# Kernel optimization log

Measured on AMD Instinct MI355X. Metric: run time of the kernel, lower is better.

## Reference

```python
import jax, jax.numpy as jnp
import numpy as np

N, E, T, D, C = 20000, 160000, 3, 128, 128  # nodes, edges, replicas, in=out feat dim, num_classes
NUM_EDGES = 128  # linear1 output width (must be <= C for the H scatter to be in-range)


def setup_inputs() -> dict:
    key = jax.random.key(0)
    ks = jax.random.split(key, 8)
    s = 1.0 / np.sqrt(D)
    return {
        "edge_index": jax.random.randint(ks[0], (2, E), 0, N, dtype=jnp.int32),
        "features": jax.random.normal(ks[1], (N, D), jnp.float32),
        "lin_W": jax.random.normal(ks[2], (T, D, D), jnp.float32) * s,   # t per-replica Linears
        "lin_b": jnp.zeros((T, D), jnp.float32),
        "gcn1_W": jax.random.normal(ks[3], (D, C), jnp.float32) * s,
        "gcn1_b": jnp.zeros((C,), jnp.float32),
        "gcn2_W": jax.random.normal(ks[4], (C, C), jnp.float32) * s,
        "gcn2_b": jnp.zeros((C,), jnp.float32),
        "lin1_W": jax.random.normal(ks[5], (C, NUM_EDGES), jnp.float32) * s,
        "lin1_b": jnp.zeros((NUM_EDGES,), jnp.float32),
    }


def _gcn(x, W, b, src, dst, n):
    """PyG GCNConv: add self-loops, symmetric deg^-1/2 normalization, scatter-add."""
    loop = jnp.arange(n, dtype=src.dtype)
    src = jnp.concatenate([src, loop])
    dst = jnp.concatenate([dst, loop])
    deg = jax.ops.segment_sum(jnp.ones(src.shape, x.dtype), dst, num_segments=n)
    dinv = jax.lax.rsqrt(deg)  # deg >= 1 because of self-loops
    norm = dinv[src] * dinv[dst]
    xw = x @ W
    return jax.ops.segment_sum(xw[src] * norm[:, None], dst, num_segments=n) + b


def reference(edge_index, features, lin_W, lin_b, gcn1_W, gcn1_b, gcn2_W, gcn2_b, lin1_W, lin1_b):
    src, dst = edge_index[0], edge_index[1]
    n = features.shape[0]
    t = lin_W.shape[0]
    scale = features.shape[1] ** -0.5  # out_features ** -0.5
    # t linear replicas, concatenated along nodes -> [t*n, D]
    transformed = (jnp.einsum('nd,tde->tne', features, lin_W) + lin_b[:, None, :]).reshape(t * n, -1)
    # replicate-selection via cosine similarity (exact torch index order:
    # src.repeat_interleave(t) vs dst.repeat(t))
    rep_src = jnp.repeat(src, t)
    exp_dst = jnp.tile(dst, t)
    a = features[rep_src]
    bb = transformed[exp_dst]
    sim = (a * bb).sum(-1) / jnp.maximum(
        jnp.linalg.norm(a, axis=-1) * jnp.linalg.norm(bb, axis=-1), 1e-8)
    best = jnp.argmax(sim.reshape(-1, t), axis=1)            # [E]
    best_nodes = dst + best.astype(dst.dtype) * n            # index into replica blocks
    # extra edges: (arange(n), arange(n) + i*n) for i in range(t)
    extra_src = jnp.tile(jnp.arange(n, dtype=src.dtype), t)
    extra_dst = (jnp.arange(n, dtype=src.dtype)[None, :]
                 + (jnp.arange(t, dtype=src.dtype) * n)[:, None]).reshape(-1)
    src_all = jnp.concatenate([src, src, extra_src])
    dst_all = jnp.concatenate([dst, best_nodes, extra_dst])
    nt = (t + 1) * n
    all_features = jnp.concatenate([features, transformed], axis=0)  # [(t+1)n, D]
    # GCN backbone (dropout = identity in eval mode)
    h = jax.nn.relu(all_features)
    h = jax.nn.relu(_gcn(h, gcn1_W, gcn1_b, src_all, dst_all, nt))
    all_features2 = _gcn(h, gcn2_W, gcn2_b, src_all, dst_all, nt)    # [(t+1)n, C]
    logits = jax.nn.relu(all_features2) @ lin1_W + lin1_b            # [(t+1)n, NUM_EDGES]
    num_classes = gcn2_b.shape[0]
    classes = jnp.argmax(logits.reshape(t + 1, n, -1), axis=-1)      # [t+1, n]
    H = jax.nn.one_hot(classes, num_classes, dtype=features.dtype).sum(0)  # [n, C] vote counts
    # per-class segment sum over nodes with H[:, j] > 0 (only first n rows are ever selected)
    mask = (H > 0).astype(features.dtype)                            # [n, C]
    hyperedge_features = mask.T @ all_features2[:n]                  # [C, D]
    dots = (all_features @ hyperedge_features.T) * scale             # [(t+1)n, C]
    H = jax.nn.softmax(H, axis=0)
    return H, hyperedge_features, dots
```

## Files before the change

kernel.cpp:

```cpp
#include <hip/hip_runtime.h>
#include <math.h>

#define NN 20000
#define NE 160000
#define TT 3
#define DD 128
#define NTOT 80000
#define N3 60000
#define NBLK1 79

__device__ __forceinline__ float waveReduceSum(float v) {
#pragma unroll
  for (int off = 32; off >= 1; off >>= 1)
    v += __shfl_xor(v, off, 64);
  return v;
}

__device__ __forceinline__ void atomAddF(float* p, float v) {
  unsafeAtomicAdd(p, v);
}

__global__ __launch_bounds__(256) void k_copy_feat(const float* __restrict__ src,
                                                   float* __restrict__ dst, int n4) {
  int i = blockIdx.x * 256 + threadIdx.x;
  if (i < n4) ((float4*)dst)[i] = ((const float4*)src)[i];
}

template <int RELU_IN, int TRANS_W, int DO_ARGMAX>
__global__ __launch_bounds__(512, 4) void gemm128(const float* __restrict__ X,
                                                  const float* __restrict__ W,
                                                  const float* __restrict__ bias,
                                                  float* __restrict__ out, int M,
                                                  float scale, int wStride, int bStride,
                                                  long oStride, int* __restrict__ cls) {
  __shared__ float Ws[128 * 132];
  const int tid = threadIdx.x;
  const int rbase = blockIdx.x * 160;
  W += (long)blockIdx.y * wStride;
  if (bias) bias += (long)blockIdx.y * bStride;
  out += (long)blockIdx.y * oStride;

#pragma unroll
  for (int it = 0; it < 8; ++it) {
    int idx = (tid + it * 512) * 4;
    int kl = idx >> 7, c = idx & 127;
    float4 w;
    if (!TRANS_W) {
      w = *(const float4*)&W[kl * 128 + c];
    } else {
      w.x = W[(c + 0) * 128 + kl];
      w.y = W[(c + 1) * 128 + kl];
      w.z = W[(c + 2) * 128 + kl];
      w.w = W[(c + 3) * 128 + kl];
    }
    *(float4*)&Ws[kl * 132 + c] = w;
  }

  const int tc = tid & 15, tr = tid >> 4;
  const int c0 = tc * 8, r0 = tr * 5;

  const float4* xrow[5];
#pragma unroll
  for (int i = 0; i < 5; ++i) {
    int gr = rbase + r0 + i;
    int gc = (gr < M) ? gr : 0;
    xrow[i] = (const float4*)(X + (long)gc * 128);
  }

  float acc[5][8];
#pragma unroll
  for (int i = 0; i < 5; ++i)
#pragma unroll
    for (int j = 0; j < 8; ++j) acc[i][j] = 0.f;

  float4 xc[5], xn[5];
#pragma unroll
  for (int i = 0; i < 5; ++i) {
    float4 v = xrow[i][0];
    if (RELU_IN) {
      v.x = fmaxf(v.x, 0.f);
      v.y = fmaxf(v.y, 0.f);
      v.z = fmaxf(v.z, 0.f);
      v.w = fmaxf(v.w, 0.f);
    }
    xc[i] = v;
  }

  __syncthreads();

  for (int kq = 0; kq < 32; ++kq) {
    if (kq < 31) {
#pragma unroll
      for (int i = 0; i < 5; ++i) {
        float4 v = xrow[i][kq + 1];
        if (RELU_IN) {
          v.x = fmaxf(v.x, 0.f);
          v.y = fmaxf(v.y, 0.f);
          v.z = fmaxf(v.z, 0.f);
          v.w = fmaxf(v.w, 0.f);
        }
        xn[i] = v;
      }
    }
    const int klb = kq * 4;
#pragma unroll
    for (int k = 0; k < 4; ++k) {
      const int kl = klb + k;
      const float4 wa = *(const float4*)&Ws[kl * 132 + c0];
      const float4 wb = *(const float4*)&Ws[kl * 132 + c0 + 4];
      float av[5];
#pragma unroll
      for (int i = 0; i < 5; ++i)
        av[i] = (k == 0) ? xc[i].x : (k == 1) ? xc[i].y : (k == 2) ? xc[i].z : xc[i].w;
      const float bv[8] = {wa.x, wa.y, wa.z, wa.w, wb.x, wb.y, wb.z, wb.w};
#pragma unroll
      for (int i = 0; i < 5; ++i)
#pragma unroll
        for (int j = 0; j < 8; ++j) acc[i][j] = fmaf(av[i], bv[j], acc[i][j]);
    }
    if (kq < 31) {
#pragma unroll
      for (int i = 0; i < 5; ++i) xc[i] = xn[i];
    }
  }

  float bb[8];
#pragma unroll
  for (int j = 0; j < 8; ++j) bb[j] = 0.f;
  if (bias) {
#pragma unroll
    for (int j = 0; j < 8; ++j) bb[j] = bias[c0 + j];
  }

  if (DO_ARGMAX) {
#pragma unroll
    for (int i = 0; i < 5; ++i) {
      float bv = acc[i][0] * scale + bb[0];
      int bc = c0;
#pragma unroll
      for (int j = 1; j < 8; ++j) {
        float v = acc[i][j] * scale + bb[j];
        if (v > bv) {
          bv = v;
          bc = c0 + j;
        }
      }
#pragma unroll
      for (int off = 1; off <= 8; off <<= 1) {
        float ov = __shfl_xor(bv, off, 64);
        int oc = __shfl_xor(bc, off, 64);
        if (ov > bv || (ov == bv && oc < bc)) {
          bv = ov;
          bc = oc;
        }
      }
      int gr = rbase + r0 + i;
      if (tc == 0 && gr < M) cls[gr] = bc;
    }
  } else {
#pragma unroll
    for (int i = 0; i < 5; ++i) {
      int gr = rbase + r0 + i;
      if (gr < M) {
        float4 v0, v1;
        v0.x = acc[i][0] * scale + bb[0];
        v0.y = acc[i][1] * scale + bb[1];
        v0.z = acc[i][2] * scale + bb[2];
        v0.w = acc[i][3] * scale + bb[3];
        v1.x = acc[i][4] * scale + bb[4];
        v1.y = acc[i][5] * scale + bb[5];
        v1.z = acc[i][6] * scale + bb[6];
        v1.w = acc[i][7] * scale + bb[7];
        *(float4*)&out[(long)gr * 128 + c0] = v0;
        *(float4*)&out[(long)gr * 128 + c0 + 4] = v1;
      }
    }
  }
}

__global__ __launch_bounds__(256) void k_norms(const float* __restrict__ feat,
                                               const float* __restrict__ A,
                                               float* __restrict__ nf,
                                               float* __restrict__ nt0) {
  int w = blockIdx.x * 4 + (threadIdx.x >> 6);
  int lane = threadIdx.x & 63;
  if (w >= 2 * NN) return;
  const float* p = (w < NN) ? (feat + (long)w * 128) : (A + (long)(NN + (w - NN)) * 128);
  float2 v = *(const float2*)(p + lane * 2);
  float s = waveReduceSum(v.x * v.x + v.y * v.y);
  if (lane == 0) {
    float r = sqrtf(s);
    if (w < NN) nf[w] = r;
    else nt0[w - NN] = r;
  }
}

__global__ __launch_bounds__(256) void k_sim(const int* __restrict__ ei,
                                             const float* __restrict__ feat,
                                             const float* __restrict__ A,
                                             const float* __restrict__ nf,
                                             const float* __restrict__ nt0,
                                             int* __restrict__ bn) {
  int e = blockIdx.x * 4 + (threadIdx.x >> 6);
  int lane = threadIdx.x & 63;
  if (e >= NE) return;
  int s = ei[e];
  float2 a = *(const float2*)(feat + (long)s * 128 + lane * 2);
  float na = nf[s];
  int dd[3];
#pragma unroll
  for (int k = 0; k < 3; ++k) {
    int j = 3 * e + k;
    if (j >= NE) j -= NE;
    if (j >= NE) j -= NE;
    dd[k] = ei[NE + j];
  }
  float2 b0 = *(const float2*)(A + (long)(NN + dd[0]) * 128 + lane * 2);
  float2 b1 = *(const float2*)(A + (long)(NN + dd[1]) * 128 + lane * 2);
  float2 b2 = *(const float2*)(A + (long)(NN + dd[2]) * 128 + lane * 2);
  float s0 = waveReduceSum(a.x * b0.x + a.y * b0.y);
  float s1 = waveReduceSum(a.x * b1.x + a.y * b1.y);
  float s2 = waveReduceSum(a.x * b2.x + a.y * b2.y);
  float sim0 = s0 / fmaxf(na * nt0[dd[0]], 1e-8f);
  float sim1 = s1 / fmaxf(na * nt0[dd[1]], 1e-8f);
  float sim2 = s2 / fmaxf(na * nt0[dd[2]], 1e-8f);
  int bk = 0;
  float bv = sim0;
  if (sim1 > bv) {
    bv = sim1;
    bk = 1;
  }
  if (sim2 > bv) {
    bv = sim2;
    bk = 2;
  }
  if (lane == 0) bn[e] = ei[NE + e] + bk * NN;
}

__global__ __launch_bounds__(256) void k_zero_count(int* __restrict__ count) {
  int v = blockIdx.x * 256 + threadIdx.x;
  if (v < NTOT) count[v] = 0;
}

__global__ __launch_bounds__(256) void k_count(const int* __restrict__ ei,
                                               const int* __restrict__ bn,
                                               int* __restrict__ count) {
  int e = blockIdx.x * 256 + threadIdx.x;
  if (e < NE) {
    atomicAdd(&count[ei[NE + e]], 1);
    atomicAdd(&count[bn[e]], 1);
  }
}

__global__ __launch_bounds__(256) void k_dinv(const int* __restrict__ count,
                                              float* __restrict__ dinv) {
  int v = blockIdx.x * 256 + threadIdx.x;
  if (v < NTOT) {
    float deg = (float)count[v] + ((v < N3) ? 2.f : 1.f);
    dinv[v] = 1.f / sqrtf(deg);
  }
}

__global__ __launch_bounds__(256) void k_scan1(const int* __restrict__ count,
                                               int* __restrict__ start,
                                               int* __restrict__ bsum) {
  __shared__ int sh[256];
  const int b = blockIdx.x, t = threadIdx.x;
  const int base = b * 1024 + t * 4;
  int c[4];
  int s = 0;
#pragma unroll
  for (int k = 0; k < 4; ++k) {
    int idx = base + k;
    c[k] = (idx < NTOT) ? count[idx] : 0;
    s += c[k];
  }
  sh[t] = s;
  __syncthreads();
  for (int off = 1; off < 256; off <<= 1) {
    int v = (t >= off) ? sh[t - off] : 0;
    __syncthreads();
    sh[t] += v;
    __syncthreads();
  }
  if (t == 255) bsum[b] = sh[255];
  int run = sh[t] - s;
#pragma unroll
  for (int k = 0; k < 4; ++k) {
    int idx = base + k;
    if (idx < NTOT) start[idx] = run;
    run += c[k];
  }
}

__global__ __launch_bounds__(256) void k_scan2(int* __restrict__ bsum) {
  __shared__ int sh[256];
  const int t = threadIdx.x;
  int v = (t < NBLK1) ? bsum[t] : 0;
  sh[t] = v;
  __syncthreads();
  for (int off = 1; off < 256; off <<= 1) {
    int u = (t >= off) ? sh[t - off] : 0;
    __syncthreads();
    sh[t] += u;
    __syncthreads();
  }
  if (t < NBLK1) bsum[t] = sh[t] - v;
}

__global__ __launch_bounds__(256) void k_scan3(int* __restrict__ start,
                                               const int* __restrict__ bsum,
                                               int* __restrict__ cursor) {
  int i = blockIdx.x * 256 + threadIdx.x;
  if (i < NTOT) {
    int v = start[i] + bsum[i >> 10];
    start[i] = v;
    cursor[i] = v;
  }
}

__global__ __launch_bounds__(256) void k_fill(const int* __restrict__ ei,
                                              const int* __restrict__ bn,
                                              const float* __restrict__ dinv,
                                              int* __restrict__ cursor,
                                              int2* __restrict__ ent) {
  int g = blockIdx.x * 256 + threadIdx.x;
  if (g >= 2 * NE) return;
  int e = (g < NE) ? g : g - NE;
  int s = ei[e];
  int d = (g < NE) ? ei[NE + e] : bn[e];
  float w = dinv[s] * dinv[d];
  int pos = atomicAdd(&cursor[d], 1);
  ent[pos] = make_int2(s, __float_as_int(w));
}

__global__ __launch_bounds__(256) void k_agg(const int2* __restrict__ ent,
                                             const int* __restrict__ start,
                                             const int* __restrict__ end,
                                             const float* __restrict__ xw,
                                             const float* __restrict__ dinv,
                                             const float* __restrict__ bias,
                                             float* __restrict__ out) {
  int v = blockIdx.x * 4 + (threadIdx.x >> 6);
  int lane = threadIdx.x & 63;
  float dv = dinv[v];
  float2 xv = *(const float2*)(xw + (long)v * 128 + lane * 2);
  float2 b2 = *(const float2*)(bias + lane * 2);
  float acc0 = b2.x + dv * dv * xv.x;
  float acc1 = b2.y + dv * dv * xv.y;
  if (v < NN) {
    acc0 += dv * dv * xv.x;
    acc1 += dv * dv * xv.y;
  } else if (v < N3) {
    int j = (v < 2 * NN) ? v - NN : v - 2 * NN;
    float2 xj = *(const float2*)(xw + (long)j * 128 + lane * 2);
    float w = dinv[j] * dv;
    acc0 = fmaf(w, xj.x, acc0);
    acc1 = fmaf(w, xj.y, acc1);
  }
  const int i1 = end[v];
  int i = start[v];
  for (; i + 1 < i1; i += 2) {
    int2 e0 = ent[i], e1 = ent[i + 1];
    float w0 = __int_as_float(e0.y), w1 = __int_as_float(e1.y);
    float2 x0 = *(const float2*)(xw + (long)e0.x * 128 + lane * 2);
    float2 x1 = *(const float2*)(xw + (long)e1.x * 128 + lane * 2);
    acc0 = fmaf(w0, x0.x, acc0);
    acc1 = fmaf(w0, x0.y, acc1);
    acc0 = fmaf(w1, x1.x, acc0);
    acc1 = fmaf(w1, x1.y, acc1);
  }
  if (i < i1) {
    int2 e0 = ent[i];
    float w0 = __int_as_float(e0.y);
    float2 x0 = *(const float2*)(xw + (long)e0.x * 128 + lane * 2);
    acc0 = fmaf(w0, x0.x, acc0);
    acc1 = fmaf(w0, x0.y, acc1);
  }
  *(float2*)(out + (long)v * 128 + lane * 2) = make_float2(acc0, acc1);
}

__global__ __launch_bounds__(256) void k_zero_small(float* __restrict__ hyper,
                                                    int* __restrict__ hist) {
  int i = blockIdx.x * 256 + threadIdx.x;
  if (i < 128 * 128) hyper[i] = 0.f;
  if (i < 640) hist[i] = 0;
}

#define HISTBLK 20
__global__ __launch_bounds__(256) void k_hist(const int* __restrict__ cls,
                                              int* __restrict__ hist) {
  __shared__ int sh[640];
  const int t = threadIdx.x;
  for (int i = t; i < 640; i += 256) sh[i] = 0;
  __syncthreads();
  const int per = NN / HISTBLK;
  const int j0 = blockIdx.x * per;
  for (int j = j0 + t; j < j0 + per; j += 256) {
    int cc[4] = {cls[j], cls[NN + j], cls[2 * NN + j], cls[3 * NN + j]};
#pragma unroll
    for (int i = 0; i < 4; ++i) {
      bool first = true;
      int m = 0;
#pragma unroll
      for (int k = 0; k < 4; ++k) {
        if (cc[k] == cc[i]) {
          if (k < i) first = false;
          m++;
        }
      }
      if (first) atomicAdd(&sh[cc[i] * 5 + m], 1);
    }
  }
  __syncthreads();
  for (int i = t; i < 640; i += 256) {
    int v = sh[i];
    if (v) atomicAdd(&hist[i], v);
  }
}

__global__ void k_table(const int* __restrict__ hist, float* __restrict__ table) {
  int c = threadIdx.x;
  if (c >= 128) return;
  int cnt[5];
  int tot = 0;
  for (int v = 1; v <= 4; ++v) {
    cnt[v] = hist[c * 5 + v];
    tot += cnt[v];
  }
  cnt[0] = NN - tot;
  int m = 0;
  for (int v = 0; v <= 4; ++v)
    if (cnt[v] > 0) m = v;
  float ex[5];
  float denom = 0.f;
  for (int v = 0; v <= 4; ++v) {
    ex[v] = expf((float)(v - m));
    denom += (float)cnt[v] * ex[v];
  }
  for (int v = 0; v <= 4; ++v) table[c * 5 + v] = ex[v] / denom;
}

__global__ __launch_bounds__(256) void k_hwrite(const int* __restrict__ cls,
                                                const float* __restrict__ table,
                                                float* __restrict__ H) {
  int j = blockIdx.x * 2 + (threadIdx.x >> 7);
  int c = threadIdx.x & 127;
  if (j >= NN) return;
  int c0 = cls[j], c1 = cls[NN + j], c2 = cls[2 * NN + j], c3 = cls[3 * NN + j];
  int cnt = (c == c0) + (c == c1) + (c == c2) + (c == c3);
  H[(long)j * 128 + c] = table[c * 5 + cnt];
}

#define HBLK 250
#define HPER 80
__global__ __launch_bounds__(256) void k_hyper(const int* __restrict__ cls,
                                               const float* __restrict__ af2,
                                               float* __restrict__ hyper) {
  __shared__ float acc[128 * 128];
  const int t = threadIdx.x;
  for (int i = t; i < 128 * 128; i += 256) acc[i] = 0.f;
  __syncthreads();
  const int j0 = blockIdx.x * HPER;
  const int j1 = j0 + HPER;
  const int d = t & 127;
  const int half = t >> 7;
  float v = af2[(long)j0 * 128 + d];
  int c0 = cls[j0], c1 = cls[NN + j0], c2 = cls[2 * NN + j0], c3 = cls[3 * NN + j0];
  for (int j = j0; j < j1; ++j) {
    float vn = 0.f;
    int n0 = 0, n1 = 0, n2 = 0, n3 = 0;
    if (j + 1 < j1) {
      vn = af2[(long)(j + 1) * 128 + d];
      n0 = cls[j + 1];
      n1 = cls[NN + j + 1];
      n2 = cls[2 * NN + j + 1];
      n3 = cls[3 * NN + j + 1];
    }
    if (half == 0) {
      atomicAdd(&acc[c0 * 128 + d], v);
      if (c2 != c0 && c2 != c1) atomicAdd(&acc[c2 * 128 + d], v);
    } else {
      if (c1 != c0) atomicAdd(&acc[c1 * 128 + d], v);
      if (c3 != c0 && c3 != c1 && c3 != c2) atomicAdd(&acc[c3 * 128 + d], v);
    }
    v = vn;
    c0 = n0;
    c1 = n1;
    c2 = n2;
    c3 = n3;
  }
  __syncthreads();
  for (int i = t; i < 128 * 128; i += 256) {
    float x = acc[i];
    if (x != 0.f) atomAddF(&hyper[i], x);
  }
}

extern "C" void kernel_launch(void* const* d_in, const int* in_sizes, int n_in,
                              void* d_out, int out_size, void* d_ws, size_t ws_size,
                              hipStream_t stream) {
  (void)in_sizes;
  (void)n_in;
  (void)out_size;
  (void)ws_size;
  const int* ei = (const int*)d_in[0];
  const float* feat = (const float*)d_in[1];
  const float* lin_W = (const float*)d_in[2];
  const float* lin_b = (const float*)d_in[3];
  const float* g1W = (const float*)d_in[4];
  const float* g1b = (const float*)d_in[5];
  const float* g2W = (const float*)d_in[6];
  const float* g2b = (const float*)d_in[7];
  const float* l1W = (const float*)d_in[8];
  const float* l1b = (const float*)d_in[9];

  float* out = (float*)d_out;
  float* H = out;
  float* hyper = out + (size_t)NN * 128;
  float* dots = hyper + 128 * 128;

  float* ws = (float*)d_ws;
  float* A = ws;
  float* Cb = A + (size_t)NTOT * 128;
  float* Bb = dots;
  float* dinv = Cb + (size_t)NTOT * 128;
  float* nf = dinv + NTOT;
  float* nt0 = nf + NN;
  int* bn = (int*)(nt0 + NN);
  int* cls = bn + NE;
  int* hist = cls + NTOT;
  float* table = (float*)(hist + 640);
  int* count = (int*)(table + 640);
  int* startA = count + NTOT;
  int* cursor = startA + NTOT;
  int* bsum = cursor + NTOT;
  int2* ent = (int2*)(bsum + 128);

  const float kScale = 0.08838834764831843f;

  k_copy_feat<<<(NN * 128 / 4 + 255) / 256, 256, 0, stream>>>(feat, A, NN * 128 / 4);
  gemm128<0, 0, 0><<<dim3(125, 3), 512, 0, stream>>>(
      feat, lin_W, lin_b, A + (size_t)NN * 128, NN, 1.f, 128 * 128, 128,
      (long)NN * 128, nullptr);
  k_norms<<<10000, 256, 0, stream>>>(feat, A, nf, nt0);
  k_zero_count<<<(NTOT + 255) / 256, 256, 0, stream>>>(count);
  k_sim<<<NE / 4, 256, 0, stream>>>(ei, feat, A, nf, nt0, bn);
  k_count<<<(NE + 255) / 256, 256, 0, stream>>>(ei, bn, count);
  k_dinv<<<(NTOT + 255) / 256, 256, 0, stream>>>(count, dinv);
  k_scan1<<<NBLK1, 256, 0, stream>>>(count, startA, bsum);
  k_scan2<<<1, 256, 0, stream>>>(bsum);
  k_scan3<<<(NTOT + 255) / 256, 256, 0, stream>>>(startA, bsum, cursor);
  k_fill<<<(2 * NE + 255) / 256, 256, 0, stream>>>(ei, bn, dinv, cursor, ent);
  gemm128<1, 0, 0><<<dim3(NTOT / 160, 1), 512, 0, stream>>>(A, g1W, nullptr, Bb, NTOT,
                                                            1.f, 0, 0, 0, nullptr);
  k_agg<<<NTOT / 4, 256, 0, stream>>>(ent, startA, cursor, Bb, dinv, g1b, Cb);
  gemm128<1, 0, 0><<<dim3(NTOT / 160, 1), 512, 0, stream>>>(Cb, g2W, nullptr, Bb, NTOT,
                                                            1.f, 0, 0, 0, nullptr);
  k_agg<<<NTOT / 4, 256, 0, stream>>>(ent, startA, cursor, Bb, dinv, g2b, Cb);
  gemm128<1, 0, 1><<<dim3(NTOT / 160, 1), 512, 0, stream>>>(Cb, l1W, l1b, nullptr,
                                                            NTOT, 1.f, 0, 0, 0, cls);
  k_zero_small<<<64, 256, 0, stream>>>(hyper, hist);
  k_hist<<<HISTBLK, 256, 0, stream>>>(cls, hist);
  k_table<<<1, 128, 0, stream>>>(hist, table);
  k_hwrite<<<NN / 2, 256, 0, stream>>>(cls, table, H);
  k_hyper<<<HBLK, 256, 0, stream>>>(cls, Cb, hyper);
  gemm128<0, 1, 0><<<dim3(NTOT / 160, 1), 512, 0, stream>>>(A, hyper, nullptr, dots,
                                                            NTOT, kScale, 0, 0, 0,
                                                            nullptr);
}
```

Measured before the change: 468.0 us.

## Process two edges per wave in k_sim with register prefetch of next edge

Rewrites the similarity kernel so each 64-lane wave handles two edges (one per half-wave) using float4 loads. Each wave loops over four edges with software-pipelined prefetch of the next edge's gathers. This is meant to raise memory-level parallelism on the random gathers and cut wave count. The gemm launch-bound occupancy hint also changes from 4 to 3 blocks, which may allow more registers per thread but fewer resident blocks.

```diff
diff --git a/kernel.cpp b/kernel.cpp
--- a/kernel.cpp
+++ b/kernel.cpp
@@ -8,6 +8,7 @@
 #define NTOT 80000
 #define N3 60000
 #define NBLK1 79
+#define SIMW 20000
 
 __device__ __forceinline__ float waveReduceSum(float v) {
 #pragma unroll
@@ -27,7 +28,7 @@
 }
 
 template <int RELU_IN, int TRANS_W, int DO_ARGMAX>
-__global__ __launch_bounds__(512, 4) void gemm128(const float* __restrict__ X,
+__global__ __launch_bounds__(512, 3) void gemm128(const float* __restrict__ X,
                                                   const float* __restrict__ W,
                                                   const float* __restrict__ bias,
                                                   float* __restrict__ out, int M,
@@ -201,40 +202,84 @@
                                              const float* __restrict__ nf,
                                              const float* __restrict__ nt0,
                                              int* __restrict__ bn) {
-  int e = blockIdx.x * 4 + (threadIdx.x >> 6);
-  int lane = threadIdx.x & 63;
-  if (e >= NE) return;
-  int s = ei[e];
-  float2 a = *(const float2*)(feat + (long)s * 128 + lane * 2);
-  float na = nf[s];
-  int dd[3];
-#pragma unroll
-  for (int k = 0; k < 3; ++k) {
-    int j = 3 * e + k;
-    if (j >= NE) j -= NE;
-    if (j >= NE) j -= NE;
-    dd[k] = ei[NE + j];
-  }
-  float2 b0 = *(const float2*)(A + (long)(NN + dd[0]) * 128 + lane * 2);
-  float2 b1 = *(const float2*)(A + (long)(NN + dd[1]) * 128 + lane * 2);
-  float2 b2 = *(const float2*)(A + (long)(NN + dd[2]) * 128 + lane * 2);
-  float s0 = waveReduceSum(a.x * b0.x + a.y * b0.y);
-  float s1 = waveReduceSum(a.x * b1.x + a.y * b1.y);
-  float s2 = waveReduceSum(a.x * b2.x + a.y * b2.y);
-  float sim0 = s0 / fmaxf(na * nt0[dd[0]], 1e-8f);
-  float sim1 = s1 / fmaxf(na * nt0[dd[1]], 1e-8f);
-  float sim2 = s2 / fmaxf(na * nt0[dd[2]], 1e-8f);
-  int bk = 0;
-  float bv = sim0;
-  if (sim1 > bv) {
-    bv = sim1;
-    bk = 1;
-  }
-  if (sim2 > bv) {
-    bv = sim2;
-    bk = 2;
-  }
-  if (lane == 0) bn[e] = ei[NE + e] + bk * NN;
+  const int t = threadIdx.x;
+  const int lane = t & 31;
+  const int half = (t >> 5) & 1;
+  const int w = blockIdx.x * 4 + (t >> 6);
+
+#define SIM_LOAD(I, E, DE, AV, B0, B1, B2, NA, NB0, NB1, NB2)              \
+  {                                                                        \
+    E = 2 * (w + (I)*SIMW) + half;                                         \
+    DE = ei[NE + E];                                                       \
+    int s_ = ei[E];                                                        \
+    int j0_ = 3 * E;                                                       \
+    if (j0_ >= NE) j0_ -= NE;                                              \
+    if (j0_ >= NE) j0_ -= NE;                                              \
+    int j1_ = j0_ + 1;                                                     \
+    if (j1_ >= NE) j1_ -= NE;                                              \
+    int j2_ = j0_ + 2;                                                     \
+    if (j2_ >= NE) j2_ -= NE;                                              \
+    int d0_ = ei[NE + j0_], d1_ = ei[NE + j1_], d2_ = ei[NE + j2_];        \
+    AV = ((const float4*)(feat + (long)s_ * 128))[lane];                   \
+    B0 = ((const float4*)(A + (long)(NN + d0_) * 128))[lane];              \
+    B1 = ((const float4*)(A + (long)(NN + d1_) * 128))[lane];              \
+    B2 = ((const float4*)(A + (long)(NN + d2_) * 128))[lane];              \
+    NA = nf[s_];                                                           \
+    NB0 = nt0[d0_];                                                        \
+    NB1 = nt0[d1_];                                                        \
+    NB2 = nt0[d2_];                                                        \
+  }
+
+  int ec, dec;
+  float4 ac, b0c, b1c, b2c;
+  float nac, nb0c, nb1c, nb2c;
+  SIM_LOAD(0, ec, dec, ac, b0c, b1c, b2c, nac, nb0c, nb1c, nb2c);
+
+#pragma unroll
+  for (int i = 0; i < 4; ++i) {
+    int en = 0, den = 0;
+    float4 an, b0n, b1n, b2n;
+    float nan2 = 0.f, nb0n = 0.f, nb1n = 0.f, nb2n = 0.f;
+    if (i < 3) {
+      SIM_LOAD(i + 1, en, den, an, b0n, b1n, b2n, nan2, nb0n, nb1n, nb2n);
+    }
+    float p0 = ac.x * b0c.x + ac.y * b0c.y + ac.z * b0c.z + ac.w * b0c.w;
+    float p1 = ac.x * b1c.x + ac.y * b1c.y + ac.z * b1c.z + ac.w * b1c.w;
+    float p2 = ac.x * b2c.x + ac.y * b2c.y + ac.z * b2c.z + ac.w * b2c.w;
+#pragma unroll
+    for (int off = 1; off <= 16; off <<= 1) {
+      p0 += __shfl_xor(p0, off, 64);
+      p1 += __shfl_xor(p1, off, 64);
+      p2 += __shfl_xor(p2, off, 64);
+    }
+    float s0 = p0 / fmaxf(nac * nb0c, 1e-8f);
+    float s1 = p1 / fmaxf(nac * nb1c, 1e-8f);
+    float s2 = p2 / fmaxf(nac * nb2c, 1e-8f);
+    int bk = 0;
+    float bv = s0;
+    if (s1 > bv) {
+      bv = s1;
+      bk = 1;
+    }
+    if (s2 > bv) {
+      bv = s2;
+      bk = 2;
+    }
+    if (lane == 0) bn[ec] = dec + bk * NN;
+    if (i < 3) {
+      ec = en;
+      dec = den;
+      ac = an;
+      b0c = b0n;
+      b1c = b1n;
+      b2c = b2n;
+      nac = nan2;
+      nb0c = nb0n;
+      nb1c = nb1n;
+      nb2c = nb2n;
+    }
+  }
+#undef SIM_LOAD
 }
 
 __global__ __launch_bounds__(256) void k_zero_count(int* __restrict__ count) {
@@ -545,7 +590,7 @@
       (long)NN * 128, nullptr);
   k_norms<<<10000, 256, 0, stream>>>(feat, A, nf, nt0);
   k_zero_count<<<(NTOT + 255) / 256, 256, 0, stream>>>(count);
-  k_sim<<<NE / 4, 256, 0, stream>>>(ei, feat, A, nf, nt0, bn);
+  k_sim<<<SIMW / 4, 256, 0, stream>>>(ei, feat, A, nf, nt0, bn);
   k_count<<<(NE + 255) / 256, 256, 0, stream>>>(ei, bn, count);
   k_dinv<<<(NTOT + 255) / 256, 256, 0, stream>>>(count, dinv);
   k_scan1<<<NBLK1, 256, 0, stream>>>(count, startA, bsum);
```

New measurement: 435.7 us. -6.9%, faster.
